# Kernel optimization log

Measured on AMD Instinct MI355X. Metric: run time of the kernel, lower is better.

The kernel has to match this reference:

```python
import jax, jax.numpy as jnp
import numpy as np

B, S, HID, H, HKV, HD = 2, 1024, 4096, 32, 8, 128
NEG = -1e9
W_STD = 0.02


def _rotary(q, k, pos):
    # NeoX-style rotate-half rotary embedding, theta=10000
    inv_freq = 1.0 / (10000.0 ** (jnp.arange(0, HD, 2, dtype=jnp.float32) / HD))  # [HD/2]
    ang = pos[..., None].astype(jnp.float32) * inv_freq            # [B,S,HD/2]
    cos = jnp.concatenate([jnp.cos(ang), jnp.cos(ang)], -1)[:, :, None, :]  # [B,S,1,HD]
    sin = jnp.concatenate([jnp.sin(ang), jnp.sin(ang)], -1)[:, :, None, :]

    def rot_half(t):
        h1, h2 = jnp.split(t, 2, axis=-1)
        return jnp.concatenate([-h2, h1], axis=-1)

    return q * cos + rot_half(q) * sin, k * cos + rot_half(k) * sin


def setup_inputs() -> dict:
    key = jax.random.key(0)
    ks = jax.random.split(key, 6)
    x = jax.random.normal(ks[0], (B * S, HID), jnp.float32)
    wq = jax.random.normal(ks[1], (HID, H * HD), jnp.float32) * W_STD
    wk = jax.random.normal(ks[2], (HID, HKV * HD), jnp.float32) * W_STD
    wv = jax.random.normal(ks[3], (HID, HKV * HD), jnp.float32) * W_STD
    wo = jax.random.normal(ks[4], (H * HD, HID), jnp.float32) * W_STD
    # additive causal mask (module uses is_causal=False and an explicit attn_mask)
    attn_mask = jnp.where(jnp.triu(jnp.ones((S, S), bool), 1), NEG, 0.0).astype(jnp.float32)
    return {
        "x": x,
        "attn_mask": attn_mask,
        "wq": wq, "wk": wk, "wv": wv, "wo": wo,
        "seqstarts": jnp.arange(B + 1, dtype=jnp.int32) * S,
        "kvstarts": jnp.arange(B + 1, dtype=jnp.int32) * S,
        "cachestarts": jnp.arange(B, dtype=jnp.int32) * S,
        "decoding_batches": 0,
        "start_pos": jnp.zeros((B,), jnp.int32),
        "max_seqlen": S,
        "max_kvlen": S,
        "first_seqlen": jnp.full((B,), S, jnp.int32),
        "kv_cache": jnp.zeros((1,), jnp.float32),
        "kv_scale": jnp.zeros((1,), jnp.float32),
    }


def reference(x, attn_mask, wq, wk, wv, wo, seqstarts, kvstarts, cachestarts,
              decoding_batches, start_pos, max_seqlen, max_kvlen, first_seqlen,
              kv_cache, kv_scale):
    # QKV projections on flattened ragged tokens (uniform seqlens -> dense [B,S])
    xq = (x @ wq).reshape(B, S, H, HD)
    xk = (x @ wk).reshape(B, S, HKV, HD)
    xv = (x @ wv).reshape(B, S, HKV, HD)
    pos = start_pos[:, None] + jnp.arange(S, dtype=jnp.int32)  # [B,S]
    xq, xk = _rotary(xq, xk, pos)
    # GQA: repeat kv heads (friendly_gqa path of key_value_cache, num_repeat=4)
    g = H // HKV
    k = jnp.repeat(xk, g, axis=2)  # [B,S,H,HD]
    v = jnp.repeat(xv, g, axis=2)
    scale = 1.0 / jnp.sqrt(jnp.float32(HD))
    scores = jnp.einsum('bqhd,bkhd->bhqk', xq, k) * scale + attn_mask  # [B,H,S,S]
    p = jax.nn.softmax(scores, axis=-1)
    attn = jnp.einsum('bhqk,bkhd->bqhd', p, v).reshape(B * S, H * HD)
    return attn @ wo
```

## Files before the change

kernel.cpp:

```cpp
#include <hip/hip_runtime.h>
#include <hip/hip_bf16.h>

#define B_    2
#define S_    1024
#define HID_  4096
#define H_    32
#define HKV_  8
#define HD_   128

typedef __attribute__((ext_vector_type(8))) short   bf16x8_t;
typedef __attribute__((ext_vector_type(4))) float   f32x4_t;

__device__ __forceinline__ unsigned short f2bf(float f) {
    union { float f; unsigned u; } v; v.f = f;
    unsigned r = v.u + 0x7fffu + ((v.u >> 16) & 1u);
    return (unsigned short)(r >> 16);
}
__device__ __forceinline__ float bf2f(unsigned short u) {
    union { unsigned u; float f; } v; v.u = ((unsigned)u) << 16;
    return v.f;
}

__device__ __forceinline__ void gload_lds16(const void* g, void* l) {
    __builtin_amdgcn_global_load_lds(
        (const __attribute__((address_space(1))) unsigned int*)g,
        (__attribute__((address_space(3))) unsigned int*)l, 16, 0, 0);
}

__global__ __launch_bounds__(256) void cvt_f32_bf16(const float* __restrict__ in,
                                                    unsigned short* __restrict__ out,
                                                    int n4) {
    int i = blockIdx.x * 256 + threadIdx.x;
    if (i >= n4) return;
    float4 v = reinterpret_cast<const float4*>(in)[i];
    uint2 p;
    p.x = (unsigned)f2bf(v.x) | ((unsigned)f2bf(v.y) << 16);
    p.y = (unsigned)f2bf(v.z) | ((unsigned)f2bf(v.w) << 16);
    reinterpret_cast<uint2*>(out)[i] = p;
}

__global__ __launch_bounds__(256) void tcvt(const float* __restrict__ W,
                                            unsigned short* __restrict__ Wt,
                                            int ldW, int Kdim) {
    __shared__ unsigned short L[32][36];
    const int t = threadIdx.x;
    const int kb = blockIdx.y, nb = blockIdx.x;
    {
        int kr = t >> 3, nc = (t & 7) * 4;
        float4 v = *reinterpret_cast<const float4*>(&W[(size_t)(kb * 32 + kr) * ldW + nb * 32 + nc]);
        L[nc + 0][kr] = f2bf(v.x);
        L[nc + 1][kr] = f2bf(v.y);
        L[nc + 2][kr] = f2bf(v.z);
        L[nc + 3][kr] = f2bf(v.w);
    }
    __syncthreads();
    {
        int nr = t >> 3, kc = (t & 7) * 4;
        uint2 o;
        o.x = (unsigned)L[nr][kc + 0] | ((unsigned)L[nr][kc + 1] << 16);
        o.y = (unsigned)L[nr][kc + 2] | ((unsigned)L[nr][kc + 3] << 16);
        *reinterpret_cast<uint2*>(&Wt[(size_t)(nb * 32 + nr) * Kdim + kb * 32 + kc]) = o;
    }
}

template<bool OUT_BF16>
__global__ __launch_bounds__(256) void gemm_tt(
    const unsigned short* __restrict__ A,
    const unsigned short* __restrict__ Bt,
    void* __restrict__ Cm,
    int ldc, int K)
{
    __shared__ unsigned short As[128 * 32];
    __shared__ unsigned short Bs[128 * 32];
    const int tid  = threadIdx.x;
    const int lane = tid & 63;
    const int w    = tid >> 6;
    const int wm   = w >> 1, wn = w & 1;
    const int r    = lane & 15, g = lane >> 4;
    const int m0   = blockIdx.y * 128, n0 = blockIdx.x * 128;

    const int c0 = w * 128 + lane;
    const int c1 = c0 + 64;
    const int r0 = c0 >> 2, col0 = (c0 & 3) << 3;
    const int r1 = c1 >> 2, col1 = (c1 & 3) << 3;

    const f32x4_t zero = {0.f, 0.f, 0.f, 0.f};
    f32x4_t acc[4][4];
#pragma unroll
    for (int i = 0; i < 4; ++i)
#pragma unroll
        for (int j = 0; j < 4; ++j) acc[i][j] = zero;

    for (int k0 = 0; k0 < K; k0 += 32) {
        __syncthreads();
        gload_lds16(&A [(size_t)(m0 + r0) * K + k0 + col0], As + (size_t)(w * 2 + 0) * 512);
        gload_lds16(&A [(size_t)(m0 + r1) * K + k0 + col1], As + (size_t)(w * 2 + 1) * 512);
        gload_lds16(&Bt[(size_t)(n0 + r0) * K + k0 + col0], Bs + (size_t)(w * 2 + 0) * 512);
        gload_lds16(&Bt[(size_t)(n0 + r1) * K + k0 + col1], Bs + (size_t)(w * 2 + 1) * 512);
        __syncthreads();

        bf16x8_t af[4], bfr[4];
#pragma unroll
        for (int m = 0; m < 4; ++m)
            af[m] = *reinterpret_cast<const bf16x8_t*>(&As[(wm * 64 + m * 16 + r) * 32 + g * 8]);
#pragma unroll
        for (int n = 0; n < 4; ++n)
            bfr[n] = *reinterpret_cast<const bf16x8_t*>(&Bs[(wn * 64 + n * 16 + r) * 32 + g * 8]);
#pragma unroll
        for (int m = 0; m < 4; ++m)
#pragma unroll
            for (int n = 0; n < 4; ++n)
                acc[m][n] = __builtin_amdgcn_mfma_f32_16x16x32_bf16(af[m], bfr[n], acc[m][n], 0, 0, 0);
    }

#pragma unroll
    for (int m = 0; m < 4; ++m)
#pragma unroll
        for (int n = 0; n < 4; ++n)
#pragma unroll
            for (int j = 0; j < 4; ++j) {
                int row = m0 + wm * 64 + m * 16 + g * 4 + j;
                int col = n0 + wn * 64 + n * 16 + r;
                if constexpr (OUT_BF16)
                    reinterpret_cast<unsigned short*>(Cm)[(size_t)row * ldc + col] = f2bf(acc[m][n][j]);
                else
                    reinterpret_cast<float*>(Cm)[(size_t)row * ldc + col] = acc[m][n][j];
            }
}

__global__ __launch_bounds__(256) void gemm_kv(
    const unsigned short* __restrict__ A,
    const unsigned short* __restrict__ Bt,
    unsigned short* __restrict__ Kb,
    unsigned short* __restrict__ VT,
    int K)
{
    __shared__ unsigned short As[128 * 32];
    __shared__ unsigned short Bs[128 * 32];
    const int tid  = threadIdx.x;
    const int lane = tid & 63;
    const int w    = tid >> 6;
    const int wm   = w >> 1, wn = w & 1;
    const int r    = lane & 15, g = lane >> 4;
    const int m0   = blockIdx.y * 128, n0 = blockIdx.x * 128;

    const int c0 = w * 128 + lane;
    const int c1 = c0 + 64;
    const int r0 = c0 >> 2, col0 = (c0 & 3) << 3;
    const int r1 = c1 >> 2, col1 = (c1 & 3) << 3;

    const f32x4_t zero = {0.f, 0.f, 0.f, 0.f};
    f32x4_t acc[4][4];
#pragma unroll
    for (int i = 0; i < 4; ++i)
#pragma unroll
        for (int j = 0; j < 4; ++j) acc[i][j] = zero;

    for (int k0 = 0; k0 < K; k0 += 32) {
        __syncthreads();
        gload_lds16(&A [(size_t)(m0 + r0) * K + k0 + col0], As + (size_t)(w * 2 + 0) * 512);
        gload_lds16(&A [(size_t)(m0 + r1) * K + k0 + col1], As + (size_t)(w * 2 + 1) * 512);
        gload_lds16(&Bt[(size_t)(n0 + r0) * K + k0 + col0], Bs + (size_t)(w * 2 + 0) * 512);
        gload_lds16(&Bt[(size_t)(n0 + r1) * K + k0 + col1], Bs + (size_t)(w * 2 + 1) * 512);
        __syncthreads();

        bf16x8_t af[4], bfr[4];
#pragma unroll
        for (int m = 0; m < 4; ++m)
            af[m] = *reinterpret_cast<const bf16x8_t*>(&As[(wm * 64 + m * 16 + r) * 32 + g * 8]);
#pragma unroll
        for (int n = 0; n < 4; ++n)
            bfr[n] = *reinterpret_cast<const bf16x8_t*>(&Bs[(wn * 64 + n * 16 + r) * 32 + g * 8]);
#pragma unroll
        for (int m = 0; m < 4; ++m)
#pragma unroll
            for (int n = 0; n < 4; ++n)
                acc[m][n] = __builtin_amdgcn_mfma_f32_16x16x32_bf16(af[m], bfr[n], acc[m][n], 0, 0, 0);
    }

    const bool isV = (n0 >= 1024);
#pragma unroll
    for (int m = 0; m < 4; ++m)
#pragma unroll
        for (int n = 0; n < 4; ++n) {
            int col  = n0 + wn * 64 + n * 16 + r;
            int row0 = m0 + wm * 64 + m * 16 + g * 4;
            if (!isV) {
#pragma unroll
                for (int j = 0; j < 4; ++j)
                    Kb[(size_t)(row0 + j) * 1024 + col] = f2bf(acc[m][n][j]);
            } else {
                int d = col - 1024;
                int b = row0 >> 10, tokl = row0 & 1023;
                uint2 o;
                o.x = (unsigned)f2bf(acc[m][n][0]) | ((unsigned)f2bf(acc[m][n][1]) << 16);
                o.y = (unsigned)f2bf(acc[m][n][2]) | ((unsigned)f2bf(acc[m][n][3]) << 16);
                *reinterpret_cast<uint2*>(&VT[(size_t)(b * 1024 + d) * 1024 + tokl]) = o;
            }
        }
}

__global__ __launch_bounds__(256) void rope_table_kernel(const int* __restrict__ start_pos,
                                                         float* __restrict__ tab) {
    int i = blockIdx.x * 256 + threadIdx.x;
    int d = i & 63;
    int tok = i >> 6;
    int s = tok & (S_ - 1);
    int b = tok >> 10;
    float pos = (float)(start_pos[b] + s);
    float freq = __expf(-(float)d * (9.210340371976184f / 64.f));
    float ang = pos * freq;
    tab[tok * 128 + d]      = cosf(ang);
    tab[tok * 128 + 64 + d] = sinf(ang);
}

template<int LOGH, int STRIDE>
__global__ __launch_bounds__(256) void rope_apply_kernel(unsigned short* __restrict__ t,
                                                         const float* __restrict__ tab) {
    int i = blockIdx.x * 256 + threadIdx.x;
    int d = i & 63;
    int h = (i >> 6) & ((1 << LOGH) - 1);
    int tok = i >> (6 + LOGH);
    size_t base = (size_t)tok * STRIDE + (size_t)h * 128;
    float c  = tab[tok * 128 + d];
    float sn = tab[tok * 128 + 64 + d];
    float a = bf2f(t[base + d]);
    float b = bf2f(t[base + 64 + d]);
    t[base + d]      = f2bf(a * c - b * sn);
    t[base + 64 + d] = f2bf(b * c + a * sn);
}

__global__ __launch_bounds__(64) void attn_fwd(
    const unsigned short* __restrict__ Qb,
    const unsigned short* __restrict__ Kb,
    const unsigned short* __restrict__ VT,
    unsigned short* __restrict__ Ob)
{
    const int nQT = S_ / 32;
    const int qt = nQT - 1 - blockIdx.y;
    const int h = blockIdx.x, b = blockIdx.z;
    const int kvh = h >> 2;
    const int lane = threadIdx.x;
    const int r = lane & 15, g = lane >> 4;
    __shared__ unsigned short P_lds[32][40];

    const int qrow0 = qt * 32;
    const unsigned short* Qp = Qb + ((size_t)(b * S_) + qrow0) * 4096 + h * 128;
    bf16x8_t qf[2][4];
#pragma unroll
    for (int q2 = 0; q2 < 2; ++q2)
#pragma unroll
        for (int kk = 0; kk < 4; ++kk)
            qf[q2][kk] = *reinterpret_cast<const bf16x8_t*>(
                &Qp[(size_t)(q2 * 16 + r) * 4096 + kk * 32 + g * 8]);

    const f32x4_t zero = {0.f, 0.f, 0.f, 0.f};
    f32x4_t o[2][8];
#pragma unroll
    for (int q2 = 0; q2 < 2; ++q2)
#pragma unroll
        for (int n = 0; n < 8; ++n) o[q2][n] = zero;
    float m_[2][4], s_[2][4];
#pragma unroll
    for (int q2 = 0; q2 < 2; ++q2)
#pragma unroll
        for (int j = 0; j < 4; ++j) { m_[q2][j] = -1e30f; s_[q2][j] = 0.f; }

    const float scale = 0.08838834764831845f;
    const unsigned short* Kp = Kb + (size_t)(b * S_) * 1024 + kvh * 128;
    const unsigned short* Vt = VT + ((size_t)(b * 1024) + kvh * 128) * 1024;
    const int ntiles = qt + 1;

    for (int t = 0; t < ntiles; ++t) {
        const int k0 = t << 5;
        f32x4_t sc[2][2];
        sc[0][0] = zero; sc[0][1] = zero; sc[1][0] = zero; sc[1][1] = zero;
#pragma unroll
        for (int kk = 0; kk < 4; ++kk) {
            bf16x8_t kf0 = *reinterpret_cast<const bf16x8_t*>(
                &Kp[(size_t)(k0 + r) * 1024 + kk * 32 + g * 8]);
            bf16x8_t kf1 = *reinterpret_cast<const bf16x8_t*>(
                &Kp[(size_t)(k0 + 16 + r) * 1024 + kk * 32 + g * 8]);
#pragma unroll
            for (int q2 = 0; q2 < 2; ++q2) {
                sc[q2][0] = __builtin_amdgcn_mfma_f32_16x16x32_bf16(qf[q2][kk], kf0, sc[q2][0], 0, 0, 0);
                sc[q2][1] = __builtin_amdgcn_mfma_f32_16x16x32_bf16(qf[q2][kk], kf1, sc[q2][1], 0, 0, 0);
            }
        }
        bf16x8_t vf[8];
#pragma unroll
        for (int n = 0; n < 8; ++n)
            vf[n] = *reinterpret_cast<const bf16x8_t*>(
                &Vt[(size_t)(n * 16 + r) * 1024 + k0 + g * 8]);
        float al[2][4];
#pragma unroll
        for (int q2 = 0; q2 < 2; ++q2)
#pragma unroll
            for (int j = 0; j < 4; ++j) {
                int row = qrow0 + q2 * 16 + g * 4 + j;
                float v0 = sc[q2][0][j] * scale + ((k0 + r)      > row ? -1e9f : 0.f);
                float v1 = sc[q2][1][j] * scale + ((k0 + 16 + r) > row ? -1e9f : 0.f);
                float mx = fmaxf(v0, v1);
#pragma unroll
                for (int off = 1; off < 16; off <<= 1)
                    mx = fmaxf(mx, __shfl_xor(mx, off));
                float mn = fmaxf(m_[q2][j], mx);
                al[q2][j] = __expf(m_[q2][j] - mn);
                float p0 = __expf(v0 - mn);
                float p1 = __expf(v1 - mn);
                float rs = p0 + p1;
#pragma unroll
                for (int off = 1; off < 16; off <<= 1)
                    rs += __shfl_xor(rs, off);
                s_[q2][j] = s_[q2][j] * al[q2][j] + rs;
                m_[q2][j] = mn;
                P_lds[q2 * 16 + g * 4 + j][r]      = f2bf(p0);
                P_lds[q2 * 16 + g * 4 + j][16 + r] = f2bf(p1);
            }
#pragma unroll
        for (int q2 = 0; q2 < 2; ++q2)
#pragma unroll
            for (int n = 0; n < 8; ++n)
#pragma unroll
                for (int j = 0; j < 4; ++j)
                    o[q2][n][j] *= al[q2][j];
        __syncthreads();
        bf16x8_t pa[2];
        pa[0] = *reinterpret_cast<const bf16x8_t*>(&P_lds[r][g * 8]);
        pa[1] = *reinterpret_cast<const bf16x8_t*>(&P_lds[16 + r][g * 8]);
#pragma unroll
        for (int n = 0; n < 8; ++n)
#pragma unroll
            for (int q2 = 0; q2 < 2; ++q2)
                o[q2][n] = __builtin_amdgcn_mfma_f32_16x16x32_bf16(pa[q2], vf[n], o[q2][n], 0, 0, 0);
        __syncthreads();
    }
    unsigned short* Op = Ob + ((size_t)(b * S_) + qrow0) * 4096 + h * 128;
#pragma unroll
    for (int q2 = 0; q2 < 2; ++q2)
#pragma unroll
        for (int n = 0; n < 8; ++n)
#pragma unroll
            for (int j = 0; j < 4; ++j) {
                float val = o[q2][n][j] / s_[q2][j];
                Op[(size_t)(q2 * 16 + g * 4 + j) * 4096 + n * 16 + r] = f2bf(val);
            }
}

extern "C" void kernel_launch(void* const* d_in, const int* in_sizes, int n_in,
                              void* d_out, int out_size, void* d_ws, size_t ws_size,
                              hipStream_t stream)
{
    const float* x  = (const float*)d_in[0];
    const float* wq = (const float*)d_in[2];
    const float* wk = (const float*)d_in[3];
    const float* wv = (const float*)d_in[4];
    const float* wo = (const float*)d_in[5];
    const int* start_pos = (const int*)d_in[10];

    char* ws = (char*)d_ws;
    unsigned short* xb  = (unsigned short*)(ws);
    unsigned short* qb  = (unsigned short*)(ws + (16u << 20));
    unsigned short* kb  = (unsigned short*)(ws + (32u << 20));
    unsigned short* vT  = (unsigned short*)(ws + (36u << 20));
    unsigned short* wT  = (unsigned short*)(ws + (40u << 20));
    float*          tb  = (float*)(ws + (56u << 20));
    unsigned short* ab  = xb;
    unsigned short* wqT = (unsigned short*)d_out;
    unsigned short* woT = qb;

    cvt_f32_bf16<<<8192, 256, 0, stream>>>(x, xb, (B_ * S_ * HID_) / 4);

    tcvt<<<dim3(128, 128), 256, 0, stream>>>(wq, wqT, HID_, HID_);
    gemm_tt<true><<<dim3(32, 16), 256, 0, stream>>>(xb, wqT, qb, 4096, HID_);

    tcvt<<<dim3(32, 128), 256, 0, stream>>>(wk, wT, 1024, HID_);
    tcvt<<<dim3(32, 128), 256, 0, stream>>>(wv, wT + (size_t)1024 * HID_, 1024, HID_);
    gemm_kv<<<dim3(16, 16), 256, 0, stream>>>(xb, wT, kb, vT, HID_);

    rope_table_kernel<<<512, 256, 0, stream>>>(start_pos, tb);
    rope_apply_kernel<5, 4096><<<16384, 256, 0, stream>>>(qb, tb);
    rope_apply_kernel<3, 1024><<<4096, 256, 0, stream>>>(kb, tb);

    attn_fwd<<<dim3(H_, S_ / 32, B_), 64, 0, stream>>>(qb, kb, vT, ab);

    tcvt<<<dim3(128, 128), 256, 0, stream>>>(wo, woT, HID_, HID_);
    gemm_tt<false><<<dim3(32, 16), 256, 0, stream>>>(ab, woT, (float*)d_out, 4096, HID_);
}
```

Before: 629.2 us.

## Double-buffer GEMM LDS, swizzle, XCD remap, fuse QKV GEMMs, MFMA priority

GEMM kernels now prefetch the next K tile into a second LDS buffer while computing the current one, dropping one barrier per iteration. LDS columns are XOR-swizzled to cut bank conflicts, and workgroup IDs are remapped to group tiles per XCD for L2 locality. The Q and KV projections are merged into one 768-block launch, and attention raises wave priority around MFMA sections. The changes double LDS use per block, which may lower occupancy.

```diff
diff --git a/kernel.cpp b/kernel.cpp
--- a/kernel.cpp
+++ b/kernel.cpp
@@ -70,19 +70,24 @@
     void* __restrict__ Cm,
     int ldc, int K)
 {
-    __shared__ unsigned short As[128 * 32];
-    __shared__ unsigned short Bs[128 * 32];
+    __shared__ unsigned short As[2][128 * 32];
+    __shared__ unsigned short Bs[2][128 * 32];
     const int tid  = threadIdx.x;
     const int lane = tid & 63;
     const int w    = tid >> 6;
     const int wm   = w >> 1, wn = w & 1;
     const int r    = lane & 15, g = lane >> 4;
-    const int m0   = blockIdx.y * 128, n0 = blockIdx.x * 128;
+
+    const int nwg = gridDim.x * gridDim.y;
+    const int D   = blockIdx.y * gridDim.x + blockIdx.x;
+    const int L   = (D & 7) * (nwg >> 3) + (D >> 3);
+    const int m0  = (L / gridDim.x) * 128, n0 = (L % gridDim.x) * 128;
 
     const int c0 = w * 128 + lane;
     const int c1 = c0 + 64;
-    const int r0 = c0 >> 2, col0 = (c0 & 3) << 3;
-    const int r1 = c1 >> 2, col1 = (c1 & 3) << 3;
+    const int r0 = c0 >> 2, col0 = (((c0 & 3) ^ (r0 & 3)) << 3);
+    const int r1 = c1 >> 2, col1 = (((c1 & 3) ^ (r1 & 3)) << 3);
+    const int sw = (g ^ (r & 3)) << 3;
 
     const f32x4_t zero = {0.f, 0.f, 0.f, 0.f};
     f32x4_t acc[4][4];
@@ -91,26 +96,35 @@
 #pragma unroll
         for (int j = 0; j < 4; ++j) acc[i][j] = zero;
 
+    gload_lds16(&A [(size_t)(m0 + r0) * K + col0], &As[0][(w * 2 + 0) * 512]);
+    gload_lds16(&A [(size_t)(m0 + r1) * K + col1], &As[0][(w * 2 + 1) * 512]);
+    gload_lds16(&Bt[(size_t)(n0 + r0) * K + col0], &Bs[0][(w * 2 + 0) * 512]);
+    gload_lds16(&Bt[(size_t)(n0 + r1) * K + col1], &Bs[0][(w * 2 + 1) * 512]);
+    __syncthreads();
+
+    int cur = 0;
     for (int k0 = 0; k0 < K; k0 += 32) {
-        __syncthreads();
-        gload_lds16(&A [(size_t)(m0 + r0) * K + k0 + col0], As + (size_t)(w * 2 + 0) * 512);
-        gload_lds16(&A [(size_t)(m0 + r1) * K + k0 + col1], As + (size_t)(w * 2 + 1) * 512);
-        gload_lds16(&Bt[(size_t)(n0 + r0) * K + k0 + col0], Bs + (size_t)(w * 2 + 0) * 512);
-        gload_lds16(&Bt[(size_t)(n0 + r1) * K + k0 + col1], Bs + (size_t)(w * 2 + 1) * 512);
-        __syncthreads();
-
+        if (k0 + 32 < K) {
+            const int nk = k0 + 32, nb = cur ^ 1;
+            gload_lds16(&A [(size_t)(m0 + r0) * K + nk + col0], &As[nb][(w * 2 + 0) * 512]);
+            gload_lds16(&A [(size_t)(m0 + r1) * K + nk + col1], &As[nb][(w * 2 + 1) * 512]);
+            gload_lds16(&Bt[(size_t)(n0 + r0) * K + nk + col0], &Bs[nb][(w * 2 + 0) * 512]);
+            gload_lds16(&Bt[(size_t)(n0 + r1) * K + nk + col1], &Bs[nb][(w * 2 + 1) * 512]);
+        }
         bf16x8_t af[4], bfr[4];
 #pragma unroll
         for (int m = 0; m < 4; ++m)
-            af[m] = *reinterpret_cast<const bf16x8_t*>(&As[(wm * 64 + m * 16 + r) * 32 + g * 8]);
+            af[m] = *reinterpret_cast<const bf16x8_t*>(&As[cur][(wm * 64 + m * 16 + r) * 32 + sw]);
 #pragma unroll
         for (int n = 0; n < 4; ++n)
-            bfr[n] = *reinterpret_cast<const bf16x8_t*>(&Bs[(wn * 64 + n * 16 + r) * 32 + g * 8]);
+            bfr[n] = *reinterpret_cast<const bf16x8_t*>(&Bs[cur][(wn * 64 + n * 16 + r) * 32 + sw]);
 #pragma unroll
         for (int m = 0; m < 4; ++m)
 #pragma unroll
             for (int n = 0; n < 4; ++n)
                 acc[m][n] = __builtin_amdgcn_mfma_f32_16x16x32_bf16(af[m], bfr[n], acc[m][n], 0, 0, 0);
+        __syncthreads();
+        cur ^= 1;
     }
 
 #pragma unroll
@@ -128,26 +142,36 @@
             }
 }
 
-__global__ __launch_bounds__(256) void gemm_kv(
+__global__ __launch_bounds__(256) void gemm_qkv(
     const unsigned short* __restrict__ A,
-    const unsigned short* __restrict__ Bt,
+    const unsigned short* __restrict__ BtQ,
+    const unsigned short* __restrict__ BtKV,
+    unsigned short* __restrict__ Qb,
     unsigned short* __restrict__ Kb,
     unsigned short* __restrict__ VT,
     int K)
 {
-    __shared__ unsigned short As[128 * 32];
-    __shared__ unsigned short Bs[128 * 32];
+    __shared__ unsigned short As[2][128 * 32];
+    __shared__ unsigned short Bs[2][128 * 32];
     const int tid  = threadIdx.x;
     const int lane = tid & 63;
     const int w    = tid >> 6;
     const int wm   = w >> 1, wn = w & 1;
     const int r    = lane & 15, g = lane >> 4;
-    const int m0   = blockIdx.y * 128, n0 = blockIdx.x * 128;
+
+    const int nwg = gridDim.x * gridDim.y;
+    const int D   = blockIdx.y * gridDim.x + blockIdx.x;
+    const int L   = (D & 7) * (nwg >> 3) + (D >> 3);
+    const int m0  = (L / gridDim.x) * 128, n0 = (L % gridDim.x) * 128;
+
+    const unsigned short* Brow = (n0 < 4096) ? (BtQ + (size_t)n0 * K)
+                                             : (BtKV + (size_t)(n0 - 4096) * K);
 
     const int c0 = w * 128 + lane;
     const int c1 = c0 + 64;
-    const int r0 = c0 >> 2, col0 = (c0 & 3) << 3;
-    const int r1 = c1 >> 2, col1 = (c1 & 3) << 3;
+    const int r0 = c0 >> 2, col0 = (((c0 & 3) ^ (r0 & 3)) << 3);
+    const int r1 = c1 >> 2, col1 = (((c1 & 3) ^ (r1 & 3)) << 3);
+    const int sw = (g ^ (r & 3)) << 3;
 
     const f32x4_t zero = {0.f, 0.f, 0.f, 0.f};
     f32x4_t acc[4][4];
@@ -156,41 +180,53 @@
 #pragma unroll
         for (int j = 0; j < 4; ++j) acc[i][j] = zero;
 
+    gload_lds16(&A   [(size_t)(m0 + r0) * K + col0], &As[0][(w * 2 + 0) * 512]);
+    gload_lds16(&A   [(size_t)(m0 + r1) * K + col1], &As[0][(w * 2 + 1) * 512]);
+    gload_lds16(&Brow[(size_t)r0 * K + col0],        &Bs[0][(w * 2 + 0) * 512]);
+    gload_lds16(&Brow[(size_t)r1 * K + col1],        &Bs[0][(w * 2 + 1) * 512]);
+    __syncthreads();
+
+    int cur = 0;
     for (int k0 = 0; k0 < K; k0 += 32) {
-        __syncthreads();
-        gload_lds16(&A [(size_t)(m0 + r0) * K + k0 + col0], As + (size_t)(w * 2 + 0) * 512);
-        gload_lds16(&A [(size_t)(m0 + r1) * K + k0 + col1], As + (size_t)(w * 2 + 1) * 512);
-        gload_lds16(&Bt[(size_t)(n0 + r0) * K + k0 + col0], Bs + (size_t)(w * 2 + 0) * 512);
-        gload_lds16(&Bt[(size_t)(n0 + r1) * K + k0 + col1], Bs + (size_t)(w * 2 + 1) * 512);
-        __syncthreads();
-
+        if (k0 + 32 < K) {
+            const int nk = k0 + 32, nb = cur ^ 1;
+            gload_lds16(&A   [(size_t)(m0 + r0) * K + nk + col0], &As[nb][(w * 2 + 0) * 512]);
+            gload_lds16(&A   [(size_t)(m0 + r1) * K + nk + col1], &As[nb][(w * 2 + 1) * 512]);
+            gload_lds16(&Brow[(size_t)r0 * K + nk + col0],        &Bs[nb][(w * 2 + 0) * 512]);
+            gload_lds16(&Brow[(size_t)r1 * K + nk + col1],        &Bs[nb][(w * 2 + 1) * 512]);
+        }
         bf16x8_t af[4], bfr[4];
 #pragma unroll
         for (int m = 0; m < 4; ++m)
-            af[m] = *reinterpret_cast<const bf16x8_t*>(&As[(wm * 64 + m * 16 + r) * 32 + g * 8]);
+            af[m] = *reinterpret_cast<const bf16x8_t*>(&As[cur][(wm * 64 + m * 16 + r) * 32 + sw]);
 #pragma unroll
         for (int n = 0; n < 4; ++n)
-            bfr[n] = *reinterpret_cast<const bf16x8_t*>(&Bs[(wn * 64 + n * 16 + r) * 32 + g * 8]);
+            bfr[n] = *reinterpret_cast<const bf16x8_t*>(&Bs[cur][(wn * 64 + n * 16 + r) * 32 + sw]);
 #pragma unroll
         for (int m = 0; m < 4; ++m)
 #pragma unroll
             for (int n = 0; n < 4; ++n)
                 acc[m][n] = __builtin_amdgcn_mfma_f32_16x16x32_bf16(af[m], bfr[n], acc[m][n], 0, 0, 0);
+        __syncthreads();
+        cur ^= 1;
     }
 
-    const bool isV = (n0 >= 1024);
 #pragma unroll
     for (int m = 0; m < 4; ++m)
 #pragma unroll
         for (int n = 0; n < 4; ++n) {
             int col  = n0 + wn * 64 + n * 16 + r;
             int row0 = m0 + wm * 64 + m * 16 + g * 4;
-            if (!isV) {
+            if (n0 < 4096) {
 #pragma unroll
                 for (int j = 0; j < 4; ++j)
-                    Kb[(size_t)(row0 + j) * 1024 + col] = f2bf(acc[m][n][j]);
+                    Qb[(size_t)(row0 + j) * 4096 + col] = f2bf(acc[m][n][j]);
+            } else if (n0 < 5120) {
+#pragma unroll
+                for (int j = 0; j < 4; ++j)
+                    Kb[(size_t)(row0 + j) * 1024 + (col - 4096)] = f2bf(acc[m][n][j]);
             } else {
-                int d = col - 1024;
+                int d = col - 5120;
                 int b = row0 >> 10, tokl = row0 & 1023;
                 uint2 o;
                 o.x = (unsigned)f2bf(acc[m][n][0]) | ((unsigned)f2bf(acc[m][n][1]) << 16);
@@ -275,6 +311,7 @@
         const int k0 = t << 5;
         f32x4_t sc[2][2];
         sc[0][0] = zero; sc[0][1] = zero; sc[1][0] = zero; sc[1][1] = zero;
+        __builtin_amdgcn_s_setprio(1);
 #pragma unroll
         for (int kk = 0; kk < 4; ++kk) {
             bf16x8_t kf0 = *reinterpret_cast<const bf16x8_t*>(
@@ -287,6 +324,7 @@
                 sc[q2][1] = __builtin_amdgcn_mfma_f32_16x16x32_bf16(qf[q2][kk], kf1, sc[q2][1], 0, 0, 0);
             }
         }
+        __builtin_amdgcn_s_setprio(0);
         bf16x8_t vf[8];
 #pragma unroll
         for (int n = 0; n < 8; ++n)
@@ -328,11 +366,13 @@
         bf16x8_t pa[2];
         pa[0] = *reinterpret_cast<const bf16x8_t*>(&P_lds[r][g * 8]);
         pa[1] = *reinterpret_cast<const bf16x8_t*>(&P_lds[16 + r][g * 8]);
+        __builtin_amdgcn_s_setprio(1);
 #pragma unroll
         for (int n = 0; n < 8; ++n)
 #pragma unroll
             for (int q2 = 0; q2 < 2; ++q2)
                 o[q2][n] = __builtin_amdgcn_mfma_f32_16x16x32_bf16(pa[q2], vf[n], o[q2][n], 0, 0, 0);
+        __builtin_amdgcn_s_setprio(0);
         __syncthreads();
     }
     unsigned short* Op = Ob + ((size_t)(b * S_) + qrow0) * 4096 + h * 128;
@@ -359,24 +399,23 @@
     const int* start_pos = (const int*)d_in[10];
 
     char* ws = (char*)d_ws;
-    unsigned short* xb  = (unsigned short*)(ws);
-    unsigned short* qb  = (unsigned short*)(ws + (16u << 20));
-    unsigned short* kb  = (unsigned short*)(ws + (32u << 20));
-    unsigned short* vT  = (unsigned short*)(ws + (36u << 20));
-    unsigned short* wT  = (unsigned short*)(ws + (40u << 20));
-    float*          tb  = (float*)(ws + (56u << 20));
-    unsigned short* ab  = xb;
-    unsigned short* wqT = (unsigned short*)d_out;
-    unsigned short* woT = qb;
+    unsigned short* xb   = (unsigned short*)(ws);
+    unsigned short* qb   = (unsigned short*)(ws + (16u << 20));
+    unsigned short* kb   = (unsigned short*)(ws + (32u << 20));
+    unsigned short* vT   = (unsigned short*)(ws + (36u << 20));
+    unsigned short* wkvT = (unsigned short*)(ws + (40u << 20));
+    float*          tb   = (float*)(ws + (56u << 20));
+    unsigned short* ab   = xb;
+    unsigned short* wqT  = (unsigned short*)d_out;
+    unsigned short* woT  = qb;
 
     cvt_f32_bf16<<<8192, 256, 0, stream>>>(x, xb, (B_ * S_ * HID_) / 4);
 
     tcvt<<<dim3(128, 128), 256, 0, stream>>>(wq, wqT, HID_, HID_);
-    gemm_tt<true><<<dim3(32, 16), 256, 0, stream>>>(xb, wqT, qb, 4096, HID_);
-
-    tcvt<<<dim3(32, 128), 256, 0, stream>>>(wk, wT, 1024, HID_);
-    tcvt<<<dim3(32, 128), 256, 0, stream>>>(wv, wT + (size_t)1024 * HID_, 1024, HID_);
-    gemm_kv<<<dim3(16, 16), 256, 0, stream>>>(xb, wT, kb, vT, HID_);
+    tcvt<<<dim3(32, 128), 256, 0, stream>>>(wk, wkvT, 1024, HID_);
+    tcvt<<<dim3(32, 128), 256, 0, stream>>>(wv, wkvT + (size_t)1024 * HID_, 1024, HID_);
+
+    gemm_qkv<<<dim3(48, 16), 256, 0, stream>>>(xb, wqT, wkvT, qb, kb, vT, HID_);
 
     rope_table_kernel<<<512, 256, 0, stream>>>(start_pos, tb);
     rope_apply_kernel<5, 4096><<<16384, 256, 0, stream>>>(qb, tb);
```

After: 566.8 us. -9.9%, faster.
